# Performance work log

Hardware: AMD Instinct MI355X
Metric: run time of the kernel (lower is better)

Reference implementation:

```python
import jax, jax.numpy as jnp
import numpy as np

DIM_LOC = 2
DIM_EMBED = 32
HID = 2 * DIM_EMBED  # 64, GRUCell input and hidden size
B, T = 65536, 24


def leaky(v):
    return jnp.where(v > 0, v, 0.2 * v)


def setup_inputs() -> dict:
    key = jax.random.key(0)
    ks = jax.random.split(key, 10)
    s = lambda fan: 1.0 / np.sqrt(fan)
    return {
        "x": jax.random.normal(ks[0], (B, T, DIM_LOC), dtype=jnp.float32),
        "W_loc": jax.random.uniform(ks[1], (DIM_LOC, DIM_EMBED), jnp.float32, -s(DIM_LOC), s(DIM_LOC)),
        "b_loc": jax.random.uniform(ks[2], (DIM_EMBED,), jnp.float32, -s(DIM_LOC), s(DIM_LOC)),
        "time_table": jax.random.normal(ks[3], (24, DIM_EMBED), dtype=jnp.float32),
        "W_ih": jax.random.uniform(ks[4], (3 * HID, HID), jnp.float32, -s(HID), s(HID)),
        "W_hh": jax.random.uniform(ks[5], (3 * HID, HID), jnp.float32, -s(HID), s(HID)),
        "b_ih": jax.random.uniform(ks[6], (3 * HID,), jnp.float32, -s(HID), s(HID)),
        "b_hh": jax.random.uniform(ks[7], (3 * HID,), jnp.float32, -s(HID), s(HID)),
        "W_pred": jax.random.uniform(ks[8], (HID, 1), jnp.float32, -s(HID), s(HID)),
        "b_pred": jax.random.uniform(ks[9], (1,), jnp.float32, -s(HID), s(HID)),
    }


def reference(x, W_loc, b_loc, time_table, W_ih, W_hh, b_ih, b_hh, W_pred, b_pred):
    Bn, Tn, _ = x.shape
    # location embedding + LeakyReLU(0.2): [B, T, 32]
    embed_x = leaky(jnp.einsum('btl,le->bte', x, W_loc) + b_loc)
    # time embedding + LeakyReLU(0.2) for t = 0..T-1: [T, 32]
    embed_t = leaky(time_table[:Tn])

    def gru_step(h, inp_t):
        ex_t, et_t = inp_t  # [B,32], [32]
        inp = jnp.concatenate(
            [ex_t, jnp.broadcast_to(et_t, (ex_t.shape[0], et_t.shape[0]))], axis=1)  # [B,64]
        gi = inp @ W_ih.T + b_ih   # [B, 192]
        gh = h @ W_hh.T + b_hh     # [B, 192]
        i_r, i_z, i_n = jnp.split(gi, 3, axis=1)
        h_r, h_z, h_n = jnp.split(gh, 3, axis=1)
        r = jax.nn.sigmoid(i_r + h_r)
        z = jax.nn.sigmoid(i_z + h_z)
        n = jnp.tanh(i_n + r * h_n)
        h_new = (1.0 - z) * n + z * h
        return h_new, None

    h0 = jnp.zeros((Bn, HID), dtype=x.dtype)
    xs = (jnp.transpose(embed_x, (1, 0, 2)), embed_t)  # time-major
    h_final, _ = jax.lax.scan(gru_step, h0, xs)
    out = jax.nn.sigmoid(h_final @ W_pred + b_pred)  # [B,1]
    return out.ravel()
```

## Files before the change

### kernel.cpp

```cpp
#include <hip/hip_runtime.h>
#include <hip/hip_bf16.h>

#define TN 24
#define LOG2E 1.4426950408889634f

#define WS_GIC_F   0
#define WS_WLC_F   6144
#define WS_WI_B    24960
#define WS_WHH_B   37248

typedef __attribute__((ext_vector_type(8))) short bf16x8;
typedef __attribute__((ext_vector_type(4))) float f32x4;
typedef __attribute__((ext_vector_type(2))) float f32x2;

__device__ __forceinline__ ushort bf16rn(float f) {
    uint x = __float_as_uint(f);
    return (ushort)((x + 0x7fffu + ((x >> 16) & 1u)) >> 16);
}
__device__ __forceinline__ uint cvtpk_bf16(float lo, float hi) {
    uint r;
    asm("v_cvt_pk_bf16_f32 %0, %1, %2" : "=v"(r) : "v"(lo), "v"(hi));
    return r;
}
__device__ __forceinline__ float exp2p_(float x) {
    float r; asm("v_exp_f32 %0, %1" : "=v"(r) : "v"(x)); return r;
}
__device__ __forceinline__ float exp2n_(float x) {
    float r; asm("v_exp_f32 %0, -%1" : "=v"(r) : "v"(x)); return r;
}
__device__ __forceinline__ float sigm(float v) {
    return __builtin_amdgcn_rcpf(1.0f + __expf(-v));
}

extern "C" __global__ void __launch_bounds__(256)
traj_gru_pre(const float* __restrict__ Wloc, const float* __restrict__ bloc,
             const float* __restrict__ tt, const float* __restrict__ Wih,
             const float* __restrict__ Whh, const float* __restrict__ bih,
             const float* __restrict__ bhh, float* __restrict__ ws)
{
    const int b = blockIdx.x, tid = threadIdx.x;
    if (b < 12) {
        if (tid < 64) {
            const int er = tid & 15, cp = tid >> 4;
            int g = b >> 2, a = b & 3;
            float s = (g == 2) ? 2.0f * LOG2E : LOG2E;
            const float* src = Wih + (size_t)(g * 64 + a * 16 + er) * 64 + 8 * cp;
            union { ushort u[8]; bf16x8 v; } fr;
            #pragma unroll
            for (int j = 0; j < 8; ++j) fr.u[j] = bf16rn(s * src[j]);
            *(bf16x8*)((char*)ws + WS_WI_B + ((size_t)b * 64 + tid) * 16) = fr.v;
        }
    } else if (b < 36) {
        if (tid < 64) {
            const int er = tid & 15, cp = tid >> 4;
            int t = b - 12, g = t >> 3, r = t & 7, a = r >> 1, f = r & 1;
            float s = (g == 2) ? 2.0f * LOG2E : LOG2E;
            const float* src = Whh + (size_t)(g * 64 + a * 16 + er) * 64 + 32 * f + 8 * cp;
            union { ushort u[8]; bf16x8 v; } fr;
            #pragma unroll
            for (int j = 0; j < 8; ++j) fr.u[j] = bf16rn(s * src[j]);
            *(bf16x8*)((char*)ws + WS_WHH_B + ((size_t)t * 64 + tid) * 16) = fr.v;
        }
    } else if (b < 38) {
        const int base = (b - 36) * 3072;
        for (int i = tid; i < 3072; i += 256) {
            int idx = base + i, t = idx >> 8, g = idx & 255;
            float val;
            if (g < 192) {
                float acc = bih[g] + (g < 128 ? bhh[g] : 0.0f);
                const float* ttr = tt + t * 32;
                const float* wr  = Wih + g * 64 + 32;
                #pragma unroll
                for (int k = 0; k < 32; ++k) {
                    float e = ttr[k];
                    e = fmaxf(e, 0.2f * e);
                    acc = fmaf(wr[k], e, acc);
                }
                val = acc * (g < 128 ? LOG2E : 2.0f * LOG2E);
            } else {
                val = 2.0f * LOG2E * bhh[128 + (g - 192)];
            }
            ws[WS_GIC_F + idx] = val;
        }
    } else {
        if (tid < 96) ws[WS_WLC_F + tid] = (tid < 64) ? Wloc[tid] : bloc[tid - 64];
    }
}

extern "C" __global__ void __launch_bounds__(512, 4)
traj_gru_mfma(const float* __restrict__ x, const float* __restrict__ ws,
              const float* __restrict__ Wpred, const float* __restrict__ bpred,
              float* __restrict__ out)
{
    __shared__ __align__(16) ushort Hhi[8][16][72];
    __shared__ __align__(16) char whhS[24 * 64 * 16];
    __shared__ float wlcS[96];

    const int tid  = threadIdx.x;
    const int lane = tid & 63;
    const int wid  = tid >> 6;
    const int er   = lane & 15;
    const int cp   = lane >> 4;

    for (int i = tid; i < 24 * 64; i += 512)
        *(bf16x8*)(whhS + (size_t)i * 16) =
            *(const bf16x8*)((const char*)ws + WS_WHH_B + (size_t)i * 16);
    if (tid < 96) wlcS[tid] = ws[WS_WLC_F + tid];
    __syncthreads();

    const f32x2* wlc2 = (const f32x2*)wlcS;
    const char* wib = (const char*)ws + WS_WI_B;
    ushort* Hw = &Hhi[wid][0][0];

    const long long eg = (long long)(blockIdx.x * 8 + wid) * 16 + er;
    const float* xr = x + eg * (TN * 2);

    f32x2 hold2[4][2];
    #pragma unroll
    for (int a = 0; a < 4; ++a)
        #pragma unroll
        for (int p = 0; p < 2; ++p) hold2[a][p] = (f32x2){0.0f, 0.0f};

    const f32x2 one2    = {1.0f, 1.0f};
    const f32x2 negtwo2 = {-2.0f, -2.0f};

    float2 xv = *(const float2*)(xr);

    #pragma unroll 1
    for (int t = 0; t < TN; ++t) {
        const int tn = (t + 1 < TN) ? t + 1 : TN - 1;
        float2 xv_next = *(const float2*)(xr + tn * 2);

        union { uint u[4]; bf16x8 v; } exf;
        {
            f32x2 xx = {xv.x, xv.x}, yy = {xv.y, xv.y};
            #pragma unroll
            for (int jp = 0; jp < 4; ++jp) {
                int kp = 4 * cp + jp;
                f32x2 w1 = wlc2[kp], w2 = wlc2[16 + kp], bl = wlc2[32 + kp];
                f32x2 v = __builtin_elementwise_fma(xx, w1,
                          __builtin_elementwise_fma(yy, w2, bl));
                exf.u[jp] = cvtpk_bf16(fmaxf(v.x, 0.2f * v.x), fmaxf(v.y, 0.2f * v.y));
            }
        }

        const float* gt = ws + WS_GIC_F + t * 256;
        f32x4 accR[4], accZ[4], accNi[4], accNh[4];
        #pragma unroll
        for (int a = 0; a < 4; ++a) {
            accR[a]  = *(const f32x4*)(gt + a * 16 + 4 * cp);
            accZ[a]  = *(const f32x4*)(gt + 64 + a * 16 + 4 * cp);
            accNi[a] = *(const f32x4*)(gt + 128 + a * 16 + 4 * cp);
            accNh[a] = *(const f32x4*)(gt + 192 + a * 16 + 4 * cp);
        }

        #pragma unroll
        for (int a = 0; a < 4; ++a) {
            bf16x8 wr = *(const bf16x8*)(wib + ((size_t)(a)      * 64 + lane) * 16);
            bf16x8 wz = *(const bf16x8*)(wib + ((size_t)(4 + a)  * 64 + lane) * 16);
            bf16x8 wn = *(const bf16x8*)(wib + ((size_t)(8 + a)  * 64 + lane) * 16);
            accR[a]  = __builtin_amdgcn_mfma_f32_16x16x32_bf16(wr, exf.v, accR[a], 0, 0, 0);
            accZ[a]  = __builtin_amdgcn_mfma_f32_16x16x32_bf16(wz, exf.v, accZ[a], 0, 0, 0);
            accNi[a] = __builtin_amdgcn_mfma_f32_16x16x32_bf16(wn, exf.v, accNi[a], 0, 0, 0);
        }

        if (t > 0) {
            bf16x8 hhi0 = *(const bf16x8*)&Hw[er * 72 + 8 * cp];
            bf16x8 hhi1 = *(const bf16x8*)&Hw[er * 72 + 32 + 8 * cp];
            #pragma unroll
            for (int a = 0; a < 4; ++a) {
                bf16x8 wr0 = *(const bf16x8*)(whhS + ((size_t)(a * 2 + 0) * 64 + lane) * 16);
                bf16x8 wr1 = *(const bf16x8*)(whhS + ((size_t)(a * 2 + 1) * 64 + lane) * 16);
                accR[a] = __builtin_amdgcn_mfma_f32_16x16x32_bf16(wr0, hhi0, accR[a], 0, 0, 0);
                accR[a] = __builtin_amdgcn_mfma_f32_16x16x32_bf16(wr1, hhi1, accR[a], 0, 0, 0);
                bf16x8 wz0 = *(const bf16x8*)(whhS + ((size_t)(8 + a * 2 + 0) * 64 + lane) * 16);
                bf16x8 wz1 = *(const bf16x8*)(whhS + ((size_t)(8 + a * 2 + 1) * 64 + lane) * 16);
                accZ[a] = __builtin_amdgcn_mfma_f32_16x16x32_bf16(wz0, hhi0, accZ[a], 0, 0, 0);
                accZ[a] = __builtin_amdgcn_mfma_f32_16x16x32_bf16(wz1, hhi1, accZ[a], 0, 0, 0);
                bf16x8 wn0 = *(const bf16x8*)(whhS + ((size_t)(16 + a * 2 + 0) * 64 + lane) * 16);
                bf16x8 wn1 = *(const bf16x8*)(whhS + ((size_t)(16 + a * 2 + 1) * 64 + lane) * 16);
                accNh[a] = __builtin_amdgcn_mfma_f32_16x16x32_bf16(wn0, hhi0, accNh[a], 0, 0, 0);
                accNh[a] = __builtin_amdgcn_mfma_f32_16x16x32_bf16(wn1, hhi1, accNh[a], 0, 0, 0);
            }
        }

        #pragma unroll
        for (int a = 0; a < 4; ++a) {
            uint hiw[2];
            #pragma unroll
            for (int p = 0; p < 2; ++p) {
                f32x2 aR  = {accR[a][2 * p],  accR[a][2 * p + 1]};
                f32x2 aZ  = {accZ[a][2 * p],  accZ[a][2 * p + 1]};
                f32x2 aNi = {accNi[a][2 * p], accNi[a][2 * p + 1]};
                f32x2 aNh = {accNh[a][2 * p], accNh[a][2 * p + 1]};
                f32x2 eR = {exp2n_(aR.x), exp2n_(aR.y)};
                f32x2 eZ = {exp2n_(aZ.x), exp2n_(aZ.y)};
                f32x2 dR = eR + one2;
                f32x2 dZ = eZ + one2;
                f32x2 r  = {__builtin_amdgcn_rcpf(dR.x), __builtin_amdgcn_rcpf(dR.y)};
                f32x2 z  = {__builtin_amdgcn_rcpf(dZ.x), __builtin_amdgcn_rcpf(dZ.y)};
                f32x2 np = __builtin_elementwise_fma(r, aNh, aNi);
                f32x2 e2 = {exp2p_(np.x), exp2p_(np.y)};
                f32x2 d2 = e2 + one2;
                f32x2 rc = {__builtin_amdgcn_rcpf(d2.x), __builtin_amdgcn_rcpf(d2.y)};
                f32x2 n  = __builtin_elementwise_fma(rc, negtwo2, one2);
                f32x2 hm = hold2[a][p] - n;
                f32x2 h  = __builtin_elementwise_fma(z, hm, n);
                hold2[a][p] = h;
                hiw[p] = cvtpk_bf16(h.x, h.y);
            }
            uint2 whiv = {hiw[0], hiw[1]};
            *(uint2*)&Hw[er * 72 + 16 * a + 4 * cp] = whiv;
        }

        xv = xv_next;
    }

    float part = 0.0f;
    #pragma unroll
    for (int a = 0; a < 4; ++a) {
        f32x4 wp = *(const f32x4*)(Wpred + 16 * a + 4 * cp);
        #pragma unroll
        for (int p = 0; p < 2; ++p) {
            part = fmaf(hold2[a][p].x, wp[2 * p], part);
            part = fmaf(hold2[a][p].y, wp[2 * p + 1], part);
        }
    }
    part += __shfl_xor(part, 16);
    part += __shfl_xor(part, 32);
    if (cp == 0) out[eg] = sigm(part + bpred[0]);
}

extern "C" void kernel_launch(void* const* d_in, const int* in_sizes, int n_in,
                              void* d_out, int out_size, void* d_ws, size_t ws_size,
                              hipStream_t stream) {
    const float* x     = (const float*)d_in[0];
    const float* Wloc  = (const float*)d_in[1];
    const float* bloc  = (const float*)d_in[2];
    const float* tt    = (const float*)d_in[3];
    const float* Wih   = (const float*)d_in[4];
    const float* Whh   = (const float*)d_in[5];
    const float* bih   = (const float*)d_in[6];
    const float* bhh   = (const float*)d_in[7];
    const float* Wpred = (const float*)d_in[8];
    const float* bpred = (const float*)d_in[9];
    float* out = (float*)d_out;
    float* ws  = (float*)d_ws;

    hipLaunchKernelGGL(traj_gru_pre, dim3(39), dim3(256), 0, stream,
                       Wloc, bloc, tt, Wih, Whh, bih, bhh, ws);
    hipLaunchKernelGGL(traj_gru_mfma, dim3(512), dim3(512), 0, stream,
                       x, ws, Wpred, bpred, out);
}
```

Before: 125.1 us.

## Permute gate rows so hidden state stays in registers, drop LDS round trip

Permutes the output-row order of W_ih, W_hh and the precomputed gate constants, so each lane's MFMA accumulator outputs line up with the B-operand layout the next step's recurrent MFMA needs. The hidden state is then carried as packed bf16 registers instead of being written to and read back from a per-wave LDS buffer each timestep. The input-weight fragments also move from global memory into LDS, which takes the place of the removed hidden-state buffer. The correctness of the permutation is subtle, and the extra LDS traffic for input weights may change bank pressure.

```diff
diff --git a/kernel.cpp b/kernel.cpp
--- a/kernel.cpp
+++ b/kernel.cpp
@@ -3,6 +3,7 @@
 
 #define TN 24
 #define LOG2E 1.4426950408889634f
+
 
 #define WS_GIC_F   0
 #define WS_WLC_F   6144
@@ -30,6 +31,9 @@
 }
 __device__ __forceinline__ float sigm(float v) {
     return __builtin_amdgcn_rcpf(1.0f + __expf(-v));
+}
+__device__ __forceinline__ int sigma_(int a, int rho) {
+    return 32 * (a >> 1) + 8 * (rho >> 2) + 4 * (a & 1) + (rho & 3);
 }
 
 extern "C" __global__ void __launch_bounds__(256)
@@ -44,7 +48,7 @@
             const int er = tid & 15, cp = tid >> 4;
             int g = b >> 2, a = b & 3;
             float s = (g == 2) ? 2.0f * LOG2E : LOG2E;
-            const float* src = Wih + (size_t)(g * 64 + a * 16 + er) * 64 + 8 * cp;
+            const float* src = Wih + (size_t)(g * 64 + sigma_(a, er)) * 64 + 8 * cp;
             union { ushort u[8]; bf16x8 v; } fr;
             #pragma unroll
             for (int j = 0; j < 8; ++j) fr.u[j] = bf16rn(s * src[j]);
@@ -55,7 +59,7 @@
             const int er = tid & 15, cp = tid >> 4;
             int t = b - 12, g = t >> 3, r = t & 7, a = r >> 1, f = r & 1;
             float s = (g == 2) ? 2.0f * LOG2E : LOG2E;
-            const float* src = Whh + (size_t)(g * 64 + a * 16 + er) * 64 + 32 * f + 8 * cp;
+            const float* src = Whh + (size_t)(g * 64 + sigma_(a, er)) * 64 + 32 * f + 8 * cp;
             union { ushort u[8]; bf16x8 v; } fr;
             #pragma unroll
             for (int j = 0; j < 8; ++j) fr.u[j] = bf16rn(s * src[j]);
@@ -64,9 +68,12 @@
     } else if (b < 38) {
         const int base = (b - 36) * 3072;
         for (int i = tid; i < 3072; i += 256) {
-            int idx = base + i, t = idx >> 8, g = idx & 255;
+            int idx = base + i, t = idx >> 8, s = idx & 255;
+            int blk = s >> 6, s64 = s & 63;
+            int d = sigma_(s64 >> 4, s64 & 15);
             float val;
-            if (g < 192) {
+            if (blk < 3) {
+                int g = blk * 64 + d;
                 float acc = bih[g] + (g < 128 ? bhh[g] : 0.0f);
                 const float* ttr = tt + t * 32;
                 const float* wr  = Wih + g * 64 + 32;
@@ -78,7 +85,7 @@
                 }
                 val = acc * (g < 128 ? LOG2E : 2.0f * LOG2E);
             } else {
-                val = 2.0f * LOG2E * bhh[128 + (g - 192)];
+                val = 2.0f * LOG2E * bhh[128 + d];
             }
             ws[WS_GIC_F + idx] = val;
         }
@@ -92,7 +99,7 @@
               const float* __restrict__ Wpred, const float* __restrict__ bpred,
               float* __restrict__ out)
 {
-    __shared__ __align__(16) ushort Hhi[8][16][72];
+    __shared__ __align__(16) char wiS[12 * 64 * 16];
     __shared__ __align__(16) char whhS[24 * 64 * 16];
     __shared__ float wlcS[96];
 
@@ -102,24 +109,31 @@
     const int er   = lane & 15;
     const int cp   = lane >> 4;
 
-    for (int i = tid; i < 24 * 64; i += 512)
-        *(bf16x8*)(whhS + (size_t)i * 16) =
-            *(const bf16x8*)((const char*)ws + WS_WHH_B + (size_t)i * 16);
+    for (int i = tid; i < 36 * 64; i += 512) {
+        int f = i >> 6, l = i & 63;
+        if (f < 12)
+            *(bf16x8*)(wiS + ((size_t)f * 64 + l) * 16) =
+                *(const bf16x8*)((const char*)ws + WS_WI_B + (size_t)i * 16);
+        else
+            *(bf16x8*)(whhS + ((size_t)(f - 12) * 64 + l) * 16) =
+                *(const bf16x8*)((const char*)ws + WS_WHH_B + ((size_t)(f - 12) * 64 + l) * 16);
+    }
     if (tid < 96) wlcS[tid] = ws[WS_WLC_F + tid];
     __syncthreads();
 
     const f32x2* wlc2 = (const f32x2*)wlcS;
-    const char* wib = (const char*)ws + WS_WI_B;
-    ushort* Hw = &Hhi[wid][0][0];
 
     const long long eg = (long long)(blockIdx.x * 8 + wid) * 16 + er;
     const float* xr = x + eg * (TN * 2);
 
     f32x2 hold2[4][2];
+    uint  hf[8];
     #pragma unroll
-    for (int a = 0; a < 4; ++a)
+    for (int a = 0; a < 4; ++a) {
+        hf[2 * a] = 0u; hf[2 * a + 1] = 0u;
         #pragma unroll
         for (int p = 0; p < 2; ++p) hold2[a][p] = (f32x2){0.0f, 0.0f};
+    }
 
     const f32x2 one2    = {1.0f, 1.0f};
     const f32x2 negtwo2 = {-2.0f, -2.0f};
@@ -156,37 +170,37 @@
 
         #pragma unroll
         for (int a = 0; a < 4; ++a) {
-            bf16x8 wr = *(const bf16x8*)(wib + ((size_t)(a)      * 64 + lane) * 16);
-            bf16x8 wz = *(const bf16x8*)(wib + ((size_t)(4 + a)  * 64 + lane) * 16);
-            bf16x8 wn = *(const bf16x8*)(wib + ((size_t)(8 + a)  * 64 + lane) * 16);
+            bf16x8 wr = *(const bf16x8*)(wiS + ((size_t)a * 64 + lane) * 16);
+            bf16x8 wz = *(const bf16x8*)(wiS + ((size_t)(4 + a) * 64 + lane) * 16);
+            bf16x8 wn = *(const bf16x8*)(wiS + ((size_t)(8 + a) * 64 + lane) * 16);
             accR[a]  = __builtin_amdgcn_mfma_f32_16x16x32_bf16(wr, exf.v, accR[a], 0, 0, 0);
             accZ[a]  = __builtin_amdgcn_mfma_f32_16x16x32_bf16(wz, exf.v, accZ[a], 0, 0, 0);
             accNi[a] = __builtin_amdgcn_mfma_f32_16x16x32_bf16(wn, exf.v, accNi[a], 0, 0, 0);
         }
 
         if (t > 0) {
-            bf16x8 hhi0 = *(const bf16x8*)&Hw[er * 72 + 8 * cp];
-            bf16x8 hhi1 = *(const bf16x8*)&Hw[er * 72 + 32 + 8 * cp];
+            union { uint u[4]; bf16x8 v; } h0, h1;
+            h0.u[0] = hf[0]; h0.u[1] = hf[1]; h0.u[2] = hf[2]; h0.u[3] = hf[3];
+            h1.u[0] = hf[4]; h1.u[1] = hf[5]; h1.u[2] = hf[6]; h1.u[3] = hf[7];
             #pragma unroll
             for (int a = 0; a < 4; ++a) {
                 bf16x8 wr0 = *(const bf16x8*)(whhS + ((size_t)(a * 2 + 0) * 64 + lane) * 16);
                 bf16x8 wr1 = *(const bf16x8*)(whhS + ((size_t)(a * 2 + 1) * 64 + lane) * 16);
-                accR[a] = __builtin_amdgcn_mfma_f32_16x16x32_bf16(wr0, hhi0, accR[a], 0, 0, 0);
-                accR[a] = __builtin_amdgcn_mfma_f32_16x16x32_bf16(wr1, hhi1, accR[a], 0, 0, 0);
+                accR[a] = __builtin_amdgcn_mfma_f32_16x16x32_bf16(wr0, h0.v, accR[a], 0, 0, 0);
+                accR[a] = __builtin_amdgcn_mfma_f32_16x16x32_bf16(wr1, h1.v, accR[a], 0, 0, 0);
                 bf16x8 wz0 = *(const bf16x8*)(whhS + ((size_t)(8 + a * 2 + 0) * 64 + lane) * 16);
                 bf16x8 wz1 = *(const bf16x8*)(whhS + ((size_t)(8 + a * 2 + 1) * 64 + lane) * 16);
-                accZ[a] = __builtin_amdgcn_mfma_f32_16x16x32_bf16(wz0, hhi0, accZ[a], 0, 0, 0);
-                accZ[a] = __builtin_amdgcn_mfma_f32_16x16x32_bf16(wz1, hhi1, accZ[a], 0, 0, 0);
+                accZ[a] = __builtin_amdgcn_mfma_f32_16x16x32_bf16(wz0, h0.v, accZ[a], 0, 0, 0);
+                accZ[a] = __builtin_amdgcn_mfma_f32_16x16x32_bf16(wz1, h1.v, accZ[a], 0, 0, 0);
                 bf16x8 wn0 = *(const bf16x8*)(whhS + ((size_t)(16 + a * 2 + 0) * 64 + lane) * 16);
                 bf16x8 wn1 = *(const bf16x8*)(whhS + ((size_t)(16 + a * 2 + 1) * 64 + lane) * 16);
-                accNh[a] = __builtin_amdgcn_mfma_f32_16x16x32_bf16(wn0, hhi0, accNh[a], 0, 0, 0);
-                accNh[a] = __builtin_amdgcn_mfma_f32_16x16x32_bf16(wn1, hhi1, accNh[a], 0, 0, 0);
+                accNh[a] = __builtin_amdgcn_mfma_f32_16x16x32_bf16(wn0, h0.v, accNh[a], 0, 0, 0);
+                accNh[a] = __builtin_amdgcn_mfma_f32_16x16x32_bf16(wn1, h1.v, accNh[a], 0, 0, 0);
             }
         }
 
         #pragma unroll
         for (int a = 0; a < 4; ++a) {
-            uint hiw[2];
             #pragma unroll
             for (int p = 0; p < 2; ++p) {
                 f32x2 aR  = {accR[a][2 * p],  accR[a][2 * p + 1]};
@@ -207,10 +221,8 @@
                 f32x2 hm = hold2[a][p] - n;
                 f32x2 h  = __builtin_elementwise_fma(z, hm, n);
                 hold2[a][p] = h;
-                hiw[p] = cvtpk_bf16(h.x, h.y);
-            }
-            uint2 whiv = {hiw[0], hiw[1]};
-            *(uint2*)&Hw[er * 72 + 16 * a + 4 * cp] = whiv;
+                hf[2 * a + p] = cvtpk_bf16(h.x, h.y);
+            }
         }
 
         xv = xv_next;
@@ -219,11 +231,12 @@
     float part = 0.0f;
     #pragma unroll
     for (int a = 0; a < 4; ++a) {
-        f32x4 wp = *(const f32x4*)(Wpred + 16 * a + 4 * cp);
         #pragma unroll
         for (int p = 0; p < 2; ++p) {
-            part = fmaf(hold2[a][p].x, wp[2 * p], part);
-            part = fmaf(hold2[a][p].y, wp[2 * p + 1], part);
+            int base = 32 * (a >> 1) + 8 * cp + 4 * (a & 1) + 2 * p;
+            f32x2 wp = *(const f32x2*)(Wpred + base);
+            part = fmaf(hold2[a][p].x, wp.x, part);
+            part = fmaf(hold2[a][p].y, wp.y, part);
         }
     }
     part += __shfl_xor(part, 16);
```

After: 113.5 us. -9.2%, faster.
